# Kernel tuning notes

Hardware: AMD Instinct MI355X
Metric: run time of the kernel (lower is better)

Reference implementation:

```python
import jax, jax.numpy as jnp
import numpy as np

# Model dims (match init_kwargs)
B, N, COORD, F0 = 16, 512, 3, 64
K = 8            # kernels per layer
F1, F2 = 128, 256  # conv filters
POOL = 2
FC = 512
EPS = 1e-9


def _pairwise(C):
    """Pairwise euclidean distances D [B,N,N] and direction cosines Cos [B,N,N] from coords C [B,N,3]."""
    dot = jnp.einsum('bic,bjc->bij', C, C)
    l2 = jnp.einsum('bic,bic->bi', C, C)
    d2 = l2[:, :, None] + l2[:, None, :] - 2.0 * dot
    D = jnp.sqrt(jnp.abs(d2) + EPS)
    nrm = jnp.sqrt(l2 + EPS)
    Cos = dot / (nrm[:, :, None] * nrm[:, None, :])
    return D, Cos


def _layer(V, D, Cos, gkw, gkb, acw, acb, gcw, gcb, bng, bnb):
    """GraphKernels -> AngularContribution -> GraphConv -> tanh -> batchnorm (eval)."""
    b, n, f = V.shape
    # GraphKernels: node-dependent learned Gaussian decay over pairwise distances
    u = jax.nn.softplus(V @ gkw + gkb)                # [B,N,K]
    uk = jnp.transpose(u, (0, 2, 1))[..., None]       # [B,K,N,1]
    A = jnp.exp(-(D[:, None] ** 2) * uk)              # [B,K,N,N]
    # AngularContribution: learned interpolation between isotropic and cosine-weighted kernel
    w = jax.nn.sigmoid(V @ acw + acb)                 # [B,N,K]
    wk = jnp.transpose(w, (0, 2, 1))[..., None]       # [B,K,N,1]
    A = A * (wk * Cos[:, None] + (1.0 - wk))          # [B,K,N,N]
    # GraphConv: per-kernel message passing then shared dense over [self || messages]
    M = jnp.einsum('bkij,bjf->bikf', A, V).reshape(b, n, -1)  # [B,N,K*F]
    H = jnp.concatenate([V, M], axis=-1) @ gcw + gcb           # [B,N,F_out]
    H = jnp.tanh(H)
    # batchnorm in eval mode (moving mean 0, var 1): affine only
    return bng * H + bnb


def _pool(V, C, p):
    """AverageSeqGraphPool: average consecutive (sequence-ordered) nodes with window/stride p."""
    b, n, f = V.shape
    return V.reshape(b, n // p, p, f).mean(2), C.reshape(b, n // p, p, -1).mean(2)


def setup_inputs() -> dict:
    key = jax.random.key(0)
    ks = jax.random.split(key, 12)
    def w(k, shape):
        return jax.random.normal(k, shape, jnp.float32) / np.sqrt(shape[0])
    flat_dim = (N // POOL // POOL) * F2
    return {
        'V': jax.random.normal(ks[0], (B, N, F0), jnp.float32),
        'C': jax.random.normal(ks[1], (B, N, COORD), jnp.float32) * 10.0,  # ~Angstrom-scale coords
        'gk_w0': w(ks[2], (F0, K)), 'gk_b0': jnp.zeros((K,), jnp.float32),
        'ac_w0': w(ks[3], (F0, K)), 'ac_b0': jnp.zeros((K,), jnp.float32),
        'gc_w0': w(ks[4], ((K + 1) * F0, F1)), 'gc_b0': jnp.zeros((F1,), jnp.float32),
        'bn_g0': jnp.ones((F1,), jnp.float32), 'bn_b0': jnp.zeros((F1,), jnp.float32),
        'gk_w1': w(ks[5], (F1, K)), 'gk_b1': jnp.zeros((K,), jnp.float32),
        'ac_w1': w(ks[6], (F1, K)), 'ac_b1': jnp.zeros((K,), jnp.float32),
        'gc_w1': w(ks[7], ((K + 1) * F1, F2)), 'gc_b1': jnp.zeros((F2,), jnp.float32),
        'bn_g1': jnp.ones((F2,), jnp.float32), 'bn_b1': jnp.zeros((F2,), jnp.float32),
        'fc_w': w(ks[8], (flat_dim, FC)), 'fc_b': jnp.zeros((FC,), jnp.float32),
    }


def reference(V, C, gk_w0, gk_b0, ac_w0, ac_b0, gc_w0, gc_b0, bn_g0, bn_b0,
              gk_w1, gk_b1, ac_w1, ac_b1, gc_w1, gc_b1, bn_g1, bn_b1, fc_w, fc_b):
    D, Cos = _pairwise(C)
    H = _layer(V, D, Cos, gk_w0, gk_b0, ac_w0, ac_b0, gc_w0, gc_b0, bn_g0, bn_b0)
    H, C1 = _pool(H, C, POOL)
    D, Cos = _pairwise(C1)
    H = _layer(H, D, Cos, gk_w1, gk_b1, ac_w1, ac_b1, gc_w1, gc_b1, bn_g1, bn_b1)
    H, _ = _pool(H, C1, POOL)
    Flat = H.reshape(H.shape[0], -1)  # [B, 128*256]
    return jax.nn.sigmoid(Flat @ fc_w + fc_b)  # [B, 512]
```

## Files before the change

### kernel.cpp

```cpp
#include <hip/hip_runtime.h>
#include <math.h>

#define KK 8
#define EPSF 1e-9f

typedef unsigned int   uint32;
typedef unsigned short u16;
typedef __attribute__((ext_vector_type(8))) short bf16x8;
typedef __attribute__((ext_vector_type(4))) float f32x4;

#define MFMA_16x16x32(a, b, c) __builtin_amdgcn_mfma_f32_16x16x32_bf16(a, b, c, 0, 0, 0)

typedef __attribute__((address_space(1))) const unsigned int glob_cu32;
typedef __attribute__((address_space(3))) unsigned int lds_u32;
__device__ __forceinline__ void g2l16(const void* gsrc, void* ldst) {
    __builtin_amdgcn_global_load_lds((glob_cu32*)gsrc, (lds_u32*)ldst, 16, 0, 0);
}

__device__ __forceinline__ int swz(int row, int o) {
    return (row << 6) + (((o) ^ (row & 7)) << 3);
}

__device__ __forceinline__ float softplusf(float x) {
    return x > 0.0f ? x + log1pf(expf(-x)) : log1pf(expf(x));
}
__device__ __forceinline__ float sigmoidf_(float x) {
    return 1.0f / (1.0f + expf(-x));
}
__device__ __forceinline__ u16 f2bf(float f) {
    union { float f; uint32 u; } v; v.f = f;
    uint32 u = v.u;
    return (u16)((u + 0x7FFFu + ((u >> 16) & 1u)) >> 16);
}

__global__ __launch_bounds__(256)
void prep_kernel(const float* __restrict__ V, const float* __restrict__ W0,
                 const float* __restrict__ W1, u16* __restrict__ VT0,
                 u16* __restrict__ Wt0, u16* __restrict__ Wt1,
                 u16* __restrict__ X0) {
    __shared__ float s[64][65];
    int blk = blockIdx.x, tid = threadIdx.x;
    if (blk < 128) {
        int b = blk >> 3, rt = blk & 7;
#pragma unroll
        for (int t = 0; t < 16; t++) {
            int idx = t * 256 + tid; int r = idx >> 6, c = idx & 63;
            s[r][c] = V[((size_t)b * 512 + rt * 64 + r) * 64 + c];
        }
        __syncthreads();
#pragma unroll
        for (int t = 0; t < 16; t++) {
            int idx = t * 256 + tid; int f = idx >> 6, j = idx & 63;
            VT0[((size_t)b * 64 + f) * 512 + rt * 64 + j] = f2bf(s[j][f]);
        }
    } else if (blk < 146) {
        int t0 = blk - 128; int rt = t0 >> 1, ct = t0 & 1;
#pragma unroll
        for (int t = 0; t < 16; t++) {
            int idx = t * 256 + tid; int r = idx >> 6, c = idx & 63;
            s[r][c] = W0[((size_t)rt * 64 + r) * 128 + ct * 64 + c];
        }
        __syncthreads();
#pragma unroll
        for (int t = 0; t < 16; t++) {
            int idx = t * 256 + tid; int f = idx >> 6, j = idx & 63;
            Wt0[((size_t)ct * 64 + f) * 576 + rt * 64 + j] = f2bf(s[j][f]);
        }
    } else if (blk < 218) {
        int t0 = blk - 146; int rt = t0 >> 2, ct = t0 & 3;
#pragma unroll
        for (int t = 0; t < 16; t++) {
            int idx = t * 256 + tid; int r = idx >> 6, c = idx & 63;
            s[r][c] = W1[((size_t)rt * 64 + r) * 256 + ct * 64 + c];
        }
        __syncthreads();
#pragma unroll
        for (int t = 0; t < 16; t++) {
            int idx = t * 256 + tid; int f = idx >> 6, j = idx & 63;
            Wt1[((size_t)ct * 64 + f) * 1152 + rt * 64 + j] = f2bf(s[j][f]);
        }
    } else {
        int t0 = blk - 218;
#pragma unroll
        for (int q = 0; q < 16; q++) {
            int e = t0 * 4096 + q * 256 + tid;
            int row = e >> 6, c = e & 63;
            X0[(size_t)row * 576 + c] = f2bf(V[e]);
        }
    }
}

__global__ __launch_bounds__(256)
void t_h0p_kernel(const float* __restrict__ H0p, u16* __restrict__ VT1) {
    __shared__ float s[64][65];
    int blk = blockIdx.x, tid = threadIdx.x;
    int b = blk >> 3, rt = (blk >> 1) & 3, ct = blk & 1;
#pragma unroll
    for (int t = 0; t < 16; t++) {
        int idx = t * 256 + tid; int r = idx >> 6, c = idx & 63;
        s[r][c] = H0p[((size_t)b * 256 + rt * 64 + r) * 128 + ct * 64 + c];
    }
    __syncthreads();
#pragma unroll
    for (int t = 0; t < 16; t++) {
        int idx = t * 256 + tid; int f = idx >> 6, j = idx & 63;
        VT1[((size_t)b * 128 + ct * 64 + f) * 256 + rt * 64 + j] = f2bf(s[j][f]);
    }
}

template<int F>
__global__ __launch_bounds__(256)
void uw_kernel(const float* __restrict__ X, const float* __restrict__ gw,
               const float* __restrict__ gb, const float* __restrict__ aw,
               const float* __restrict__ ab, float* __restrict__ u,
               float* __restrict__ w, int rows) {
    int t = blockIdx.x * 256 + threadIdx.x;
    if (t >= rows * KK) return;
    int row = t >> 3, k = t & 7;
    const float4* xr = (const float4*)(X + (size_t)row * F);
    float su = 0.f, sw = 0.f;
#pragma unroll
    for (int f4 = 0; f4 < F / 4; f4++) {
        float4 x = xr[f4];
        su += x.x * gw[(f4 * 4 + 0) * 8 + k] + x.y * gw[(f4 * 4 + 1) * 8 + k]
            + x.z * gw[(f4 * 4 + 2) * 8 + k] + x.w * gw[(f4 * 4 + 3) * 8 + k];
        sw += x.x * aw[(f4 * 4 + 0) * 8 + k] + x.y * aw[(f4 * 4 + 1) * 8 + k]
            + x.z * aw[(f4 * 4 + 2) * 8 + k] + x.w * aw[(f4 * 4 + 3) * 8 + k];
    }
    u[t] = softplusf(su + gb[k]);
    w[t] = sigmoidf_(sw + ab[k]);
}

__global__ __launch_bounds__(256)
void msg0_mfma(const u16* __restrict__ VT0, const float* __restrict__ C,
               const float* __restrict__ u0, const float* __restrict__ w0,
               u16* __restrict__ X0) {
    int b = blockIdx.x >> 5, i0 = (blockIdx.x & 31) * 16;
    int tid = threadIdx.x;
    int wv = tid >> 6, lane = tid & 63, quad = lane >> 4, l15 = lane & 15;

    __shared__ __align__(16) u16 s_vT[64 * 64];
    __shared__ __align__(16) u16 s_A[128 * 64];
    __shared__ __align__(16) float s_cj[64][4];
    __shared__ __align__(16) float s_ci[16][4];
    __shared__ __align__(16) float s_u[16][KK];
    __shared__ __align__(16) float s_w[16][KK];

    if (tid < 16) {
        const float* cp = C + ((size_t)b * 512 + i0 + tid) * 3;
        float x = cp[0], y = cp[1], z = cp[2];
        s_ci[tid][0] = x; s_ci[tid][1] = y; s_ci[tid][2] = z;
        s_ci[tid][3] = x * x + y * y + z * z;
    }
    if (tid < 128) {
        int i = tid >> 3, k = tid & 7;
        size_t idx = ((size_t)b * 512 + i0 + i) * KK + k;
        s_u[i][k] = u0[idx];
        s_w[i][k] = w0[idx];
    }

    f32x4 acc[2][4] = {};

    for (int j0 = 0; j0 < 512; j0 += 64) {
        __syncthreads();
#pragma unroll
        for (int p = 0; p < 2; p++) {
            int s = p * 256 + wv * 64 + lane;
            int f = s >> 3, op = s & 7;
            g2l16(VT0 + ((size_t)b * 64 + f) * 512 + j0 + ((op ^ (f & 7)) << 3),
                  (void*)(s_vT + (p * 256 + wv * 64) * 8));
        }
        if (tid < 64) {
            const float* cp = C + ((size_t)b * 512 + j0 + tid) * 3;
            float x = cp[0], y = cp[1], z = cp[2];
            s_cj[tid][0] = x; s_cj[tid][1] = y; s_cj[tid][2] = z;
            s_cj[tid][3] = x * x + y * y + z * z;
        }
        __syncthreads();
#pragma unroll
        for (int t = 0; t < 4; t++) {
            int i = t * 4 + wv, j = lane;
            float cix = s_ci[i][0], ciy = s_ci[i][1], ciz = s_ci[i][2], l2i = s_ci[i][3];
            float cjx = s_cj[j][0], cjy = s_cj[j][1], cjz = s_cj[j][2], l2j = s_cj[j][3];
            float dot = cix * cjx + ciy * cjy + ciz * cjz;
            float d2 = fabsf(l2i + l2j - 2.f * dot) + EPSF;
            float cs = dot / sqrtf((l2i + EPSF) * (l2j + EPSF));
            f32x4 u01 = *(const f32x4*)&s_u[i][0];
            f32x4 u23 = *(const f32x4*)&s_u[i][4];
            f32x4 w01 = *(const f32x4*)&s_w[i][0];
            f32x4 w23 = *(const f32x4*)&s_w[i][4];
#pragma unroll
            for (int k = 0; k < 4; k++) {
                float a = __expf(-d2 * u01[k]) * (w01[k] * cs + 1.f - w01[k]);
                int row = i * 8 + k;
                s_A[(row << 6) + (((j >> 3) ^ (row & 7)) << 3) + (j & 7)] = f2bf(a);
            }
#pragma unroll
            for (int k = 0; k < 4; k++) {
                float a = __expf(-d2 * u23[k]) * (w23[k] * cs + 1.f - w23[k]);
                int row = i * 8 + 4 + k;
                s_A[(row << 6) + (((j >> 3) ^ (row & 7)) << 3) + (j & 7)] = f2bf(a);
            }
        }
        __syncthreads();
#pragma unroll
        for (int ks = 0; ks < 2; ks++) {
            int o = ks * 4 + quad;
            bf16x8 a0 = *(const bf16x8*)&s_A[swz(wv * 32 + l15, o)];
            bf16x8 a1 = *(const bf16x8*)&s_A[swz(wv * 32 + 16 + l15, o)];
#pragma unroll
            for (int cf = 0; cf < 4; cf++) {
                bf16x8 bv = *(const bf16x8*)&s_vT[swz(cf * 16 + l15, o)];
                acc[0][cf] = MFMA_16x16x32(a0, bv, acc[0][cf]);
                acc[1][cf] = MFMA_16x16x32(a1, bv, acc[1][cf]);
            }
        }
    }
#pragma unroll
    for (int rf = 0; rf < 2; rf++)
#pragma unroll
        for (int cf = 0; cf < 4; cf++)
#pragma unroll
            for (int r = 0; r < 4; r++) {
                int arow = wv * 32 + rf * 16 + quad * 4 + r;
                int i = arow >> 3, k = arow & 7;
                X0[((size_t)b * 512 + i0 + i) * 576 + 64 + k * 64 + cf * 16 + l15] =
                    f2bf(acc[rf][cf][r]);
            }
}

__global__ __launch_bounds__(256)
void msg1_mfma(const u16* __restrict__ VT1, const float* __restrict__ C1,
               const float* __restrict__ u1, const float* __restrict__ w1,
               u16* __restrict__ X1) {
    int b = blockIdx.x >> 4, i0 = (blockIdx.x & 15) * 16;
    int tid = threadIdx.x;
    int wv = tid >> 6, lane = tid & 63, quad = lane >> 4, l15 = lane & 15;

    __shared__ __align__(16) u16 s_vT[128 * 64];
    __shared__ __align__(16) u16 s_A[128 * 64];
    __shared__ __align__(16) float s_cj[64][4];
    __shared__ __align__(16) float s_ci[16][4];
    __shared__ __align__(16) float s_u[16][KK];
    __shared__ __align__(16) float s_w[16][KK];

    if (tid < 16) {
        const float* cp = C1 + ((size_t)b * 256 + i0 + tid) * 3;
        float x = cp[0], y = cp[1], z = cp[2];
        s_ci[tid][0] = x; s_ci[tid][1] = y; s_ci[tid][2] = z;
        s_ci[tid][3] = x * x + y * y + z * z;
    }
    if (tid < 128) {
        int i = tid >> 3, k = tid & 7;
        size_t idx = ((size_t)b * 256 + i0 + i) * KK + k;
        s_u[i][k] = u1[idx];
        s_w[i][k] = w1[idx];
    }

    f32x4 acc[2][8] = {};

    for (int j0 = 0; j0 < 256; j0 += 64) {
        __syncthreads();
#pragma unroll
        for (int p = 0; p < 4; p++) {
            int s = p * 256 + wv * 64 + lane;
            int f = s >> 3, op = s & 7;
            g2l16(VT1 + ((size_t)b * 128 + f) * 256 + j0 + ((op ^ (f & 7)) << 3),
                  (void*)(s_vT + (p * 256 + wv * 64) * 8));
        }
        if (tid < 64) {
            const float* cp = C1 + ((size_t)b * 256 + j0 + tid) * 3;
            float x = cp[0], y = cp[1], z = cp[2];
            s_cj[tid][0] = x; s_cj[tid][1] = y; s_cj[tid][2] = z;
            s_cj[tid][3] = x * x + y * y + z * z;
        }
        __syncthreads();
#pragma unroll
        for (int t = 0; t < 4; t++) {
            int i = t * 4 + wv, j = lane;
            float cix = s_ci[i][0], ciy = s_ci[i][1], ciz = s_ci[i][2], l2i = s_ci[i][3];
            float cjx = s_cj[j][0], cjy = s_cj[j][1], cjz = s_cj[j][2], l2j = s_cj[j][3];
            float dot = cix * cjx + ciy * cjy + ciz * cjz;
            float d2 = fabsf(l2i + l2j - 2.f * dot) + EPSF;
            float cs = dot / sqrtf((l2i + EPSF) * (l2j + EPSF));
            f32x4 u01 = *(const f32x4*)&s_u[i][0];
            f32x4 u23 = *(const f32x4*)&s_u[i][4];
            f32x4 w01 = *(const f32x4*)&s_w[i][0];
            f32x4 w23 = *(const f32x4*)&s_w[i][4];
#pragma unroll
            for (int k = 0; k < 4; k++) {
                float a = __expf(-d2 * u01[k]) * (w01[k] * cs + 1.f - w01[k]);
                int row = i * 8 + k;
                s_A[(row << 6) + (((j >> 3) ^ (row & 7)) << 3) + (j & 7)] = f2bf(a);
            }
#pragma unroll
            for (int k = 0; k < 4; k++) {
                float a = __expf(-d2 * u23[k]) * (w23[k] * cs + 1.f - w23[k]);
                int row = i * 8 + 4 + k;
                s_A[(row << 6) + (((j >> 3) ^ (row & 7)) << 3) + (j & 7)] = f2bf(a);
            }
        }
        __syncthreads();
#pragma unroll
        for (int ks = 0; ks < 2; ks++) {
            int o = ks * 4 + quad;
            bf16x8 a0 = *(const bf16x8*)&s_A[swz(wv * 32 + l15, o)];
            bf16x8 a1 = *(const bf16x8*)&s_A[swz(wv * 32 + 16 + l15, o)];
#pragma unroll
            for (int cf = 0; cf < 8; cf++) {
                bf16x8 bv = *(const bf16x8*)&s_vT[swz(cf * 16 + l15, o)];
                acc[0][cf] = MFMA_16x16x32(a0, bv, acc[0][cf]);
                acc[1][cf] = MFMA_16x16x32(a1, bv, acc[1][cf]);
            }
        }
    }
#pragma unroll
    for (int rf = 0; rf < 2; rf++)
#pragma unroll
        for (int cf = 0; cf < 8; cf++)
#pragma unroll
            for (int r = 0; r < 4; r++) {
                int arow = wv * 32 + rf * 16 + quad * 4 + r;
                int i = arow >> 3, k = arow & 7;
                X1[((size_t)b * 256 + i0 + i) * 1152 + 128 + k * 128 + cf * 16 + l15] =
                    f2bf(acc[rf][cf][r]);
            }
}

__global__ __launch_bounds__(256)
void post0_mfma(const u16* __restrict__ X0, const u16* __restrict__ Wt,
                const float* __restrict__ bias, const float* __restrict__ bng,
                const float* __restrict__ bnb, float* __restrict__ H0p,
                u16* __restrict__ X1) {
    int row0 = (blockIdx.x >> 1) * 32, col0 = (blockIdx.x & 1) * 64;
    int tid = threadIdx.x;
    int wv = tid >> 6, lane = tid & 63, quad = lane >> 4, l15 = lane & 15;
    int rw = wv & 1, cw = wv >> 1;

    __shared__ __align__(16) u16 s_X[32 * 64];
    __shared__ __align__(16) u16 s_W[64 * 64];

    f32x4 acc[2] = {};

    for (int kc = 0; kc < 576; kc += 64) {
        __syncthreads();
        {
            int s = wv * 64 + lane;
            int r = s >> 3, op = s & 7;
            g2l16(X0 + ((size_t)row0 + r) * 576 + kc + ((op ^ (r & 7)) << 3),
                  (void*)(s_X + (wv * 64) * 8));
        }
#pragma unroll
        for (int p = 0; p < 2; p++) {
            int s = p * 256 + wv * 64 + lane;
            int c = s >> 3, op = s & 7;
            g2l16(Wt + ((size_t)col0 + c) * 576 + kc + ((op ^ (c & 7)) << 3),
                  (void*)(s_W + (p * 256 + wv * 64) * 8));
        }
        __syncthreads();
#pragma unroll
        for (int ks = 0; ks < 2; ks++) {
            int o = ks * 4 + quad;
            bf16x8 av = *(const bf16x8*)&s_X[swz(rw * 16 + l15, o)];
#pragma unroll
            for (int cf = 0; cf < 2; cf++) {
                bf16x8 bv = *(const bf16x8*)&s_W[swz(cw * 32 + cf * 16 + l15, o)];
                acc[cf] = MFMA_16x16x32(av, bv, acc[cf]);
            }
        }
    }
#pragma unroll
    for (int cf = 0; cf < 2; cf++) {
        int col = col0 + cw * 32 + cf * 16 + l15;
        float bs = bias[col], gg = bng[col], bb = bnb[col];
        float h0 = gg * tanhf(acc[cf][0] + bs) + bb;
        float h1 = gg * tanhf(acc[cf][1] + bs) + bb;
        float h2 = gg * tanhf(acc[cf][2] + bs) + bb;
        float h3 = gg * tanhf(acc[cf][3] + bs) + bb;
        float p0 = 0.5f * (h0 + h1), p1 = 0.5f * (h2 + h3);
        size_t pr = (size_t)(row0 >> 1) + rw * 8 + quad * 2;
        H0p[pr * 128 + col] = p0;
        H0p[(pr + 1) * 128 + col] = p1;
        X1[pr * 1152 + col] = f2bf(p0);
        X1[(pr + 1) * 1152 + col] = f2bf(p1);
    }
}

__global__ __launch_bounds__(256)
void post1_mfma(const u16* __restrict__ X1, const u16* __restrict__ Wt,
                const float* __restrict__ bias, const float* __restrict__ bng,
                const float* __restrict__ bnb, float* __restrict__ H1p) {
    int row0 = (blockIdx.x >> 2) * 32, col0 = (blockIdx.x & 3) * 64;
    int tid = threadIdx.x;
    int wv = tid >> 6, lane = tid & 63, quad = lane >> 4, l15 = lane & 15;
    int rw = wv & 1, cw = wv >> 1;

    __shared__ __align__(16) u16 s_X[32 * 64];
    __shared__ __align__(16) u16 s_W[64 * 64];

    f32x4 acc[2] = {};

    for (int kc = 0; kc < 1152; kc += 64) {
        __syncthreads();
        {
            int s = wv * 64 + lane;
            int r = s >> 3, op = s & 7;
            g2l16(X1 + ((size_t)row0 + r) * 1152 + kc + ((op ^ (r & 7)) << 3),
                  (void*)(s_X + (wv * 64) * 8));
        }
#pragma unroll
        for (int p = 0; p < 2; p++) {
            int s = p * 256 + wv * 64 + lane;
            int c = s >> 3, op = s & 7;
            g2l16(Wt + ((size_t)col0 + c) * 1152 + kc + ((op ^ (c & 7)) << 3),
                  (void*)(s_W + (p * 256 + wv * 64) * 8));
        }
        __syncthreads();
#pragma unroll
        for (int ks = 0; ks < 2; ks++) {
            int o = ks * 4 + quad;
            bf16x8 av = *(const bf16x8*)&s_X[swz(rw * 16 + l15, o)];
#pragma unroll
            for (int cf = 0; cf < 2; cf++) {
                bf16x8 bv = *(const bf16x8*)&s_W[swz(cw * 32 + cf * 16 + l15, o)];
                acc[cf] = MFMA_16x16x32(av, bv, acc[cf]);
            }
        }
    }
#pragma unroll
    for (int cf = 0; cf < 2; cf++) {
        int col = col0 + cw * 32 + cf * 16 + l15;
        float bs = bias[col], gg = bng[col], bb = bnb[col];
        float h0 = gg * tanhf(acc[cf][0] + bs) + bb;
        float h1 = gg * tanhf(acc[cf][1] + bs) + bb;
        float h2 = gg * tanhf(acc[cf][2] + bs) + bb;
        float h3 = gg * tanhf(acc[cf][3] + bs) + bb;
        float p0 = 0.5f * (h0 + h1), p1 = 0.5f * (h2 + h3);
        size_t pr = (size_t)(row0 >> 1) + rw * 8 + quad * 2;
        H1p[pr * 256 + col] = p0;
        H1p[(pr + 1) * 256 + col] = p1;
    }
}

__global__ void c1pool_kernel(const float* __restrict__ C, float* __restrict__ C1) {
    int o = blockIdx.x * 256 + threadIdx.x;
    if (o >= 16 * 256 * 3) return;
    int d = o % 3;
    int node = o / 3;
    int b = node >> 8, i = node & 255;
    size_t src = ((size_t)(b * 512 + 2 * i)) * 3 + d;
    C1[o] = 0.5f * (C[src] + C[src + 3]);
}

__global__ __launch_bounds__(256)
void fc_partial_kernel(const float* __restrict__ Flat, const float* __restrict__ W,
                       float* __restrict__ P) {
    int cs = blockIdx.x & 3, ks = blockIdx.x >> 2;
    int m0 = ks * 256;
    int c4 = threadIdx.x & 31;
    int msub = threadIdx.x >> 5;

    __shared__ __align__(16) float xT[256][16];

#pragma unroll
    for (int q = 0; q < 16; q++) {
        int idx = q * 256 + threadIdx.x;
        int b = idx >> 8, mm = idx & 255;
        int bg = (b >> 2) ^ (mm & 3);
        xT[mm][(bg << 2) + (b & 3)] = Flat[(size_t)b * 32768 + m0 + mm];
    }
    __syncthreads();

    const float4* W4 = (const float4*)W;
    float4 acc[16] = {};

    for (int h = 0; h < 4; h++) {
        float4 wbuf[8];
#pragma unroll
        for (int i = 0; i < 8; i++) {
            int mm = msub * 32 + h * 8 + i;
            wbuf[i] = W4[(size_t)(m0 + mm) * 128 + cs * 32 + c4];
        }
#pragma unroll
        for (int i = 0; i < 8; i++) {
            int mm = msub * 32 + h * 8 + i;
#pragma unroll
            for (int bg = 0; bg < 4; bg++) {
                float4 xv = *(const float4*)&xT[mm][((bg ^ (mm & 3)) << 2)];
                acc[bg * 4 + 0].x += xv.x * wbuf[i].x; acc[bg * 4 + 0].y += xv.x * wbuf[i].y;
                acc[bg * 4 + 0].z += xv.x * wbuf[i].z; acc[bg * 4 + 0].w += xv.x * wbuf[i].w;
                acc[bg * 4 + 1].x += xv.y * wbuf[i].x; acc[bg * 4 + 1].y += xv.y * wbuf[i].y;
                acc[bg * 4 + 1].z += xv.y * wbuf[i].z; acc[bg * 4 + 1].w += xv.y * wbuf[i].w;
                acc[bg * 4 + 2].x += xv.z * wbuf[i].x; acc[bg * 4 + 2].y += xv.z * wbuf[i].y;
                acc[bg * 4 + 2].z += xv.z * wbuf[i].z; acc[bg * 4 + 2].w += xv.z * wbuf[i].w;
                acc[bg * 4 + 3].x += xv.w * wbuf[i].x; acc[bg * 4 + 3].y += xv.w * wbuf[i].y;
                acc[bg * 4 + 3].z += xv.w * wbuf[i].z; acc[bg * 4 + 3].w += xv.w * wbuf[i].w;
            }
        }
    }
    __syncthreads();
    __shared__ __align__(16) float red[8][32][4];
#pragma unroll
    for (int b = 0; b < 16; b++) {
        red[msub][c4][0] = acc[b].x; red[msub][c4][1] = acc[b].y;
        red[msub][c4][2] = acc[b].z; red[msub][c4][3] = acc[b].w;
        __syncthreads();
        if (msub == 0) {
            float4 s = make_float4(0.f, 0.f, 0.f, 0.f);
#pragma unroll
            for (int m = 0; m < 8; m++) {
                s.x += red[m][c4][0]; s.y += red[m][c4][1];
                s.z += red[m][c4][2]; s.w += red[m][c4][3];
            }
            *(float4*)&P[((size_t)ks * 16 + b) * 512 + cs * 128 + c4 * 4] = s;
        }
        __syncthreads();
    }
}

__global__ void fc_reduce_kernel(const float* __restrict__ P, const float* __restrict__ fcb,
                                 float* __restrict__ out) {
    int idx = blockIdx.x * 256 + threadIdx.x;
    float s0 = 0.f, s1 = 0.f;
#pragma unroll 8
    for (int ks = 0; ks < 128; ks += 2) {
        s0 += P[(size_t)ks * 8192 + idx];
        s1 += P[(size_t)(ks + 1) * 8192 + idx];
    }
    float s = s0 + s1 + fcb[idx & 511];
    out[idx] = 1.f / (1.f + expf(-s));
}

extern "C" void kernel_launch(void* const* d_in, const int* in_sizes, int n_in,
                              void* d_out, int out_size, void* d_ws, size_t ws_size,
                              hipStream_t stream) {
    const float* V     = (const float*)d_in[0];
    const float* C     = (const float*)d_in[1];
    const float* gk_w0 = (const float*)d_in[2];
    const float* gk_b0 = (const float*)d_in[3];
    const float* ac_w0 = (const float*)d_in[4];
    const float* ac_b0 = (const float*)d_in[5];
    const float* gc_w0 = (const float*)d_in[6];
    const float* gc_b0 = (const float*)d_in[7];
    const float* bn_g0 = (const float*)d_in[8];
    const float* bn_b0 = (const float*)d_in[9];
    const float* gk_w1 = (const float*)d_in[10];
    const float* gk_b1 = (const float*)d_in[11];
    const float* ac_w1 = (const float*)d_in[12];
    const float* ac_b1 = (const float*)d_in[13];
    const float* gc_w1 = (const float*)d_in[14];
    const float* gc_b1 = (const float*)d_in[15];
    const float* bn_g1 = (const float*)d_in[16];
    const float* bn_b1 = (const float*)d_in[17];
    const float* fc_w  = (const float*)d_in[18];
    const float* fc_b  = (const float*)d_in[19];
    float* out = (float*)d_out;

    float* u0  = (float*)d_ws;
    float* w0  = u0 + 65536;
    float* u1  = w0 + 65536;
    float* w1  = u1 + 32768;
    float* C1  = w1 + 32768;
    float* H0p = C1 + 12288;
    float* H1p = H0p + 524288;
    float* Pad = H1p + 524288;
    u16* X0  = (u16*)(Pad + 262144);
    u16* X1  = X0 + 4718592;
    u16* VT0 = X1 + 4718592;
    u16* Wt0 = VT0 + 524288;
    u16* Wt1 = Wt0 + 73728;
    u16* VT1 = VT0;
    float* P = (float*)X0;

    prep_kernel<<<346, 256, 0, stream>>>(V, gc_w0, gc_w1, VT0, Wt0, Wt1, X0);
    uw_kernel<64><<<256, 256, 0, stream>>>(V, gk_w0, gk_b0, ac_w0, ac_b0, u0, w0, 8192);
    msg0_mfma<<<512, 256, 0, stream>>>(VT0, C, u0, w0, X0);
    post0_mfma<<<512, 256, 0, stream>>>(X0, Wt0, gc_b0, bn_g0, bn_b0, H0p, X1);
    c1pool_kernel<<<48, 256, 0, stream>>>(C, C1);
    t_h0p_kernel<<<128, 256, 0, stream>>>(H0p, VT1);
    uw_kernel<128><<<128, 256, 0, stream>>>(H0p, gk_w1, gk_b1, ac_w1, ac_b1, u1, w1, 4096);
    msg1_mfma<<<256, 256, 0, stream>>>(VT1, C1, u1, w1, X1);
    post1_mfma<<<512, 256, 0, stream>>>(X1, Wt1, gc_b1, bn_g1, bn_b1, H1p);
    fc_partial_kernel<<<512, 256, 0, stream>>>(H1p, fc_w, P);
    fc_reduce_kernel<<<32, 256, 0, stream>>>(P, fc_b, out);
}
```

Baseline: 228.1 us.

## Fuse u/w projections and coord pooling into message kernels; split msg1 feature halves

Removes the separate uw_kernel launches and the c1pool kernel. The u/w softplus and sigmoid projections are now computed inside each message kernel's prologue, and pooled coordinates are computed on the fly from C. Per-j coordinates are loaded into registers per lane instead of being staged in shared memory, which removes one barrier per j tile. msg1 now splits its 128 features into two 64-wide halves, doubling the grid to 512 blocks and halving the accumulators. The cost is that the u/w and A-matrix work is recomputed in both feature-half blocks.

```diff
diff --git a/kernel.cpp b/kernel.cpp
--- a/kernel.cpp
+++ b/kernel.cpp
@@ -108,32 +108,11 @@
     }
 }
 
-template<int F>
-__global__ __launch_bounds__(256)
-void uw_kernel(const float* __restrict__ X, const float* __restrict__ gw,
-               const float* __restrict__ gb, const float* __restrict__ aw,
-               const float* __restrict__ ab, float* __restrict__ u,
-               float* __restrict__ w, int rows) {
-    int t = blockIdx.x * 256 + threadIdx.x;
-    if (t >= rows * KK) return;
-    int row = t >> 3, k = t & 7;
-    const float4* xr = (const float4*)(X + (size_t)row * F);
-    float su = 0.f, sw = 0.f;
-#pragma unroll
-    for (int f4 = 0; f4 < F / 4; f4++) {
-        float4 x = xr[f4];
-        su += x.x * gw[(f4 * 4 + 0) * 8 + k] + x.y * gw[(f4 * 4 + 1) * 8 + k]
-            + x.z * gw[(f4 * 4 + 2) * 8 + k] + x.w * gw[(f4 * 4 + 3) * 8 + k];
-        sw += x.x * aw[(f4 * 4 + 0) * 8 + k] + x.y * aw[(f4 * 4 + 1) * 8 + k]
-            + x.z * aw[(f4 * 4 + 2) * 8 + k] + x.w * aw[(f4 * 4 + 3) * 8 + k];
-    }
-    u[t] = softplusf(su + gb[k]);
-    w[t] = sigmoidf_(sw + ab[k]);
-}
-
 __global__ __launch_bounds__(256)
 void msg0_mfma(const u16* __restrict__ VT0, const float* __restrict__ C,
-               const float* __restrict__ u0, const float* __restrict__ w0,
+               const float* __restrict__ V,
+               const float* __restrict__ gw, const float* __restrict__ gb,
+               const float* __restrict__ aw, const float* __restrict__ ab,
                u16* __restrict__ X0) {
     int b = blockIdx.x >> 5, i0 = (blockIdx.x & 31) * 16;
     int tid = threadIdx.x;
@@ -141,27 +120,39 @@
 
     __shared__ __align__(16) u16 s_vT[64 * 64];
     __shared__ __align__(16) u16 s_A[128 * 64];
-    __shared__ __align__(16) float s_cj[64][4];
     __shared__ __align__(16) float s_ci[16][4];
     __shared__ __align__(16) float s_u[16][KK];
     __shared__ __align__(16) float s_w[16][KK];
 
+    {
+        int t = tid & 127;
+        int i = t >> 3, k = t & 7;
+        const float4* xr = (const float4*)(V + ((size_t)b * 512 + i0 + i) * 64);
+        const float* wm = (tid < 128) ? gw : aw;
+        float s = 0.f;
+#pragma unroll
+        for (int f4 = 0; f4 < 16; f4++) {
+            float4 x = xr[f4];
+            s += x.x * wm[(f4 * 4 + 0) * 8 + k] + x.y * wm[(f4 * 4 + 1) * 8 + k]
+               + x.z * wm[(f4 * 4 + 2) * 8 + k] + x.w * wm[(f4 * 4 + 3) * 8 + k];
+        }
+        if (tid < 128) s_u[i][k] = softplusf(s + gb[k]);
+        else           s_w[i][k] = sigmoidf_(s + ab[k]);
+    }
     if (tid < 16) {
         const float* cp = C + ((size_t)b * 512 + i0 + tid) * 3;
         float x = cp[0], y = cp[1], z = cp[2];
         s_ci[tid][0] = x; s_ci[tid][1] = y; s_ci[tid][2] = z;
         s_ci[tid][3] = x * x + y * y + z * z;
     }
-    if (tid < 128) {
-        int i = tid >> 3, k = tid & 7;
-        size_t idx = ((size_t)b * 512 + i0 + i) * KK + k;
-        s_u[i][k] = u0[idx];
-        s_w[i][k] = w0[idx];
-    }
+    __syncthreads();
 
     f32x4 acc[2][4] = {};
 
     for (int j0 = 0; j0 < 512; j0 += 64) {
+        const float* cp = C + ((size_t)b * 512 + j0 + lane) * 3;
+        float cjx = cp[0], cjy = cp[1], cjz = cp[2];
+        float l2j = cjx * cjx + cjy * cjy + cjz * cjz;
         __syncthreads();
 #pragma unroll
         for (int p = 0; p < 2; p++) {
@@ -170,21 +161,12 @@
             g2l16(VT0 + ((size_t)b * 64 + f) * 512 + j0 + ((op ^ (f & 7)) << 3),
                   (void*)(s_vT + (p * 256 + wv * 64) * 8));
         }
-        if (tid < 64) {
-            const float* cp = C + ((size_t)b * 512 + j0 + tid) * 3;
-            float x = cp[0], y = cp[1], z = cp[2];
-            s_cj[tid][0] = x; s_cj[tid][1] = y; s_cj[tid][2] = z;
-            s_cj[tid][3] = x * x + y * y + z * z;
-        }
-        __syncthreads();
 #pragma unroll
         for (int t = 0; t < 4; t++) {
             int i = t * 4 + wv, j = lane;
-            float cix = s_ci[i][0], ciy = s_ci[i][1], ciz = s_ci[i][2], l2i = s_ci[i][3];
-            float cjx = s_cj[j][0], cjy = s_cj[j][1], cjz = s_cj[j][2], l2j = s_cj[j][3];
-            float dot = cix * cjx + ciy * cjy + ciz * cjz;
-            float d2 = fabsf(l2i + l2j - 2.f * dot) + EPSF;
-            float cs = dot / sqrtf((l2i + EPSF) * (l2j + EPSF));
+            float dot = s_ci[i][0] * cjx + s_ci[i][1] * cjy + s_ci[i][2] * cjz;
+            float d2 = fabsf(s_ci[i][3] + l2j - 2.f * dot) + EPSF;
+            float cs = dot / sqrtf((s_ci[i][3] + EPSF) * (l2j + EPSF));
             f32x4 u01 = *(const f32x4*)&s_u[i][0];
             f32x4 u23 = *(const f32x4*)&s_u[i][4];
             f32x4 w01 = *(const f32x4*)&s_w[i][0];
@@ -230,59 +212,68 @@
 }
 
 __global__ __launch_bounds__(256)
-void msg1_mfma(const u16* __restrict__ VT1, const float* __restrict__ C1,
-               const float* __restrict__ u1, const float* __restrict__ w1,
+void msg1_mfma(const u16* __restrict__ VT1, const float* __restrict__ C,
+               const float* __restrict__ H0p,
+               const float* __restrict__ gw, const float* __restrict__ gb,
+               const float* __restrict__ aw, const float* __restrict__ ab,
                u16* __restrict__ X1) {
-    int b = blockIdx.x >> 4, i0 = (blockIdx.x & 15) * 16;
+    int b = blockIdx.x >> 5, i0 = ((blockIdx.x >> 1) & 15) * 16, fh = blockIdx.x & 1;
     int tid = threadIdx.x;
     int wv = tid >> 6, lane = tid & 63, quad = lane >> 4, l15 = lane & 15;
 
-    __shared__ __align__(16) u16 s_vT[128 * 64];
+    __shared__ __align__(16) u16 s_vT[64 * 64];
     __shared__ __align__(16) u16 s_A[128 * 64];
-    __shared__ __align__(16) float s_cj[64][4];
     __shared__ __align__(16) float s_ci[16][4];
     __shared__ __align__(16) float s_u[16][KK];
     __shared__ __align__(16) float s_w[16][KK];
 
+    {
+        int t = tid & 127;
+        int i = t >> 3, k = t & 7;
+        const float4* xr = (const float4*)(H0p + ((size_t)b * 256 + i0 + i) * 128);
+        const float* wm = (tid < 128) ? gw : aw;
+        float s = 0.f;
+#pragma unroll
+        for (int f4 = 0; f4 < 32; f4++) {
+            float4 x = xr[f4];
+            s += x.x * wm[(f4 * 4 + 0) * 8 + k] + x.y * wm[(f4 * 4 + 1) * 8 + k]
+               + x.z * wm[(f4 * 4 + 2) * 8 + k] + x.w * wm[(f4 * 4 + 3) * 8 + k];
+        }
+        if (tid < 128) s_u[i][k] = softplusf(s + gb[k]);
+        else           s_w[i][k] = sigmoidf_(s + ab[k]);
+    }
     if (tid < 16) {
-        const float* cp = C1 + ((size_t)b * 256 + i0 + tid) * 3;
-        float x = cp[0], y = cp[1], z = cp[2];
+        const float* cp = C + ((size_t)b * 512 + 2 * (i0 + tid)) * 3;
+        float x = 0.5f * (cp[0] + cp[3]);
+        float y = 0.5f * (cp[1] + cp[4]);
+        float z = 0.5f * (cp[2] + cp[5]);
         s_ci[tid][0] = x; s_ci[tid][1] = y; s_ci[tid][2] = z;
         s_ci[tid][3] = x * x + y * y + z * z;
     }
-    if (tid < 128) {
-        int i = tid >> 3, k = tid & 7;
-        size_t idx = ((size_t)b * 256 + i0 + i) * KK + k;
-        s_u[i][k] = u1[idx];
-        s_w[i][k] = w1[idx];
-    }
-
-    f32x4 acc[2][8] = {};
+    __syncthreads();
+
+    f32x4 acc[2][4] = {};
 
     for (int j0 = 0; j0 < 256; j0 += 64) {
-        __syncthreads();
-#pragma unroll
-        for (int p = 0; p < 4; p++) {
+        const float* cp = C + ((size_t)b * 512 + 2 * (j0 + lane)) * 3;
+        float cjx = 0.5f * (cp[0] + cp[3]);
+        float cjy = 0.5f * (cp[1] + cp[4]);
+        float cjz = 0.5f * (cp[2] + cp[5]);
+        float l2j = cjx * cjx + cjy * cjy + cjz * cjz;
+        __syncthreads();
+#pragma unroll
+        for (int p = 0; p < 2; p++) {
             int s = p * 256 + wv * 64 + lane;
             int f = s >> 3, op = s & 7;
-            g2l16(VT1 + ((size_t)b * 128 + f) * 256 + j0 + ((op ^ (f & 7)) << 3),
+            g2l16(VT1 + ((size_t)b * 128 + fh * 64 + f) * 256 + j0 + ((op ^ (f & 7)) << 3),
                   (void*)(s_vT + (p * 256 + wv * 64) * 8));
         }
-        if (tid < 64) {
-            const float* cp = C1 + ((size_t)b * 256 + j0 + tid) * 3;
-            float x = cp[0], y = cp[1], z = cp[2];
-            s_cj[tid][0] = x; s_cj[tid][1] = y; s_cj[tid][2] = z;
-            s_cj[tid][3] = x * x + y * y + z * z;
-        }
-        __syncthreads();
 #pragma unroll
         for (int t = 0; t < 4; t++) {
             int i = t * 4 + wv, j = lane;
-            float cix = s_ci[i][0], ciy = s_ci[i][1], ciz = s_ci[i][2], l2i = s_ci[i][3];
-            float cjx = s_cj[j][0], cjy = s_cj[j][1], cjz = s_cj[j][2], l2j = s_cj[j][3];
-            float dot = cix * cjx + ciy * cjy + ciz * cjz;
-            float d2 = fabsf(l2i + l2j - 2.f * dot) + EPSF;
-            float cs = dot / sqrtf((l2i + EPSF) * (l2j + EPSF));
+            float dot = s_ci[i][0] * cjx + s_ci[i][1] * cjy + s_ci[i][2] * cjz;
+            float d2 = fabsf(s_ci[i][3] + l2j - 2.f * dot) + EPSF;
+            float cs = dot / sqrtf((s_ci[i][3] + EPSF) * (l2j + EPSF));
             f32x4 u01 = *(const f32x4*)&s_u[i][0];
             f32x4 u23 = *(const f32x4*)&s_u[i][4];
             f32x4 w01 = *(const f32x4*)&s_w[i][0];
@@ -307,7 +298,7 @@
             bf16x8 a0 = *(const bf16x8*)&s_A[swz(wv * 32 + l15, o)];
             bf16x8 a1 = *(const bf16x8*)&s_A[swz(wv * 32 + 16 + l15, o)];
 #pragma unroll
-            for (int cf = 0; cf < 8; cf++) {
+            for (int cf = 0; cf < 4; cf++) {
                 bf16x8 bv = *(const bf16x8*)&s_vT[swz(cf * 16 + l15, o)];
                 acc[0][cf] = MFMA_16x16x32(a0, bv, acc[0][cf]);
                 acc[1][cf] = MFMA_16x16x32(a1, bv, acc[1][cf]);
@@ -317,12 +308,12 @@
 #pragma unroll
     for (int rf = 0; rf < 2; rf++)
 #pragma unroll
-        for (int cf = 0; cf < 8; cf++)
+        for (int cf = 0; cf < 4; cf++)
 #pragma unroll
             for (int r = 0; r < 4; r++) {
                 int arow = wv * 32 + rf * 16 + quad * 4 + r;
                 int i = arow >> 3, k = arow & 7;
-                X1[((size_t)b * 256 + i0 + i) * 1152 + 128 + k * 128 + cf * 16 + l15] =
+                X1[((size_t)b * 256 + i0 + i) * 1152 + 128 + k * 128 + fh * 64 + cf * 16 + l15] =
                     f2bf(acc[rf][cf][r]);
             }
 }
@@ -440,16 +431,6 @@
         H1p[pr * 256 + col] = p0;
         H1p[(pr + 1) * 256 + col] = p1;
     }
-}
-
-__global__ void c1pool_kernel(const float* __restrict__ C, float* __restrict__ C1) {
-    int o = blockIdx.x * 256 + threadIdx.x;
-    if (o >= 16 * 256 * 3) return;
-    int d = o % 3;
-    int node = o / 3;
-    int b = node >> 8, i = node & 255;
-    size_t src = ((size_t)(b * 512 + 2 * i)) * 3 + d;
-    C1[o] = 0.5f * (C[src] + C[src + 3]);
 }
 
 __global__ __launch_bounds__(256)
@@ -556,15 +537,9 @@
     const float* fc_b  = (const float*)d_in[19];
     float* out = (float*)d_out;
 
-    float* u0  = (float*)d_ws;
-    float* w0  = u0 + 65536;
-    float* u1  = w0 + 65536;
-    float* w1  = u1 + 32768;
-    float* C1  = w1 + 32768;
-    float* H0p = C1 + 12288;
+    float* H0p = (float*)d_ws;
     float* H1p = H0p + 524288;
-    float* Pad = H1p + 524288;
-    u16* X0  = (u16*)(Pad + 262144);
+    u16* X0  = (u16*)(H1p + 524288);
     u16* X1  = X0 + 4718592;
     u16* VT0 = X1 + 4718592;
     u16* Wt0 = VT0 + 524288;
@@ -573,13 +548,10 @@
     float* P = (float*)X0;
 
     prep_kernel<<<346, 256, 0, stream>>>(V, gc_w0, gc_w1, VT0, Wt0, Wt1, X0);
-    uw_kernel<64><<<256, 256, 0, stream>>>(V, gk_w0, gk_b0, ac_w0, ac_b0, u0, w0, 8192);
-    msg0_mfma<<<512, 256, 0, stream>>>(VT0, C, u0, w0, X0);
+    msg0_mfma<<<512, 256, 0, stream>>>(VT0, C, V, gk_w0, gk_b0, ac_w0, ac_b0, X0);
     post0_mfma<<<512, 256, 0, stream>>>(X0, Wt0, gc_b0, bn_g0, bn_b0, H0p, X1);
-    c1pool_kernel<<<48, 256, 0, stream>>>(C, C1);
     t_h0p_kernel<<<128, 256, 0, stream>>>(H0p, VT1);
-    uw_kernel<128><<<128, 256, 0, stream>>>(H0p, gk_w1, gk_b1, ac_w1, ac_b1, u1, w1, 4096);
-    msg1_mfma<<<256, 256, 0, stream>>>(VT1, C1, u1, w1, X1);
+    msg1_mfma<<<512, 256, 0, stream>>>(VT1, C, H0p, gk_w1, gk_b1, ac_w1, ac_b1, X1);
     post1_mfma<<<512, 256, 0, stream>>>(X1, Wt1, gc_b1, bn_g1, bn_b1, H1p);
     fc_partial_kernel<<<512, 256, 0, stream>>>(H1p, fc_w, P);
     fc_reduce_kernel<<<32, 256, 0, stream>>>(P, fc_b, out);
```

New measurement: 224.3 us. Within noise of the previous version (-1.7%).
